# Optimization experiments

Hardware: AMD Instinct MI355X
Metric: run time of the kernel (lower is better)

The kernel has to match this reference:

```python
import jax, jax.numpy as jnp
import numpy as np

N = 32768          # flattened tokens
D = 256            # latent_dim
K = 8192           # codebook_size
COMMIT_W = 0.25    # commitment_weight


def setup_inputs() -> dict:
    key = jax.random.key(0)
    k1, k2, k3 = jax.random.split(key, 3)
    x = jax.random.normal(k1, (N, D), dtype=jnp.float32)
    # nn.init.uniform_(embedding.weight, -1/K, 1/K)
    embedding = jax.random.uniform(k2, (K, D), dtype=jnp.float32,
                                   minval=-1.0 / K, maxval=1.0 / K)
    # out_proj: Linear(D, D, bias=False); torch default kaiming-uniform ~ U(-1/sqrt(D), 1/sqrt(D))
    lim = 1.0 / np.sqrt(D)
    w_out = jax.random.uniform(k3, (D, D), dtype=jnp.float32, minval=-lim, maxval=lim)
    return {"x": x, "embedding": embedding, "w_out": w_out}


def reference(x, embedding, w_out):
    sg = jax.lax.stop_gradient
    # codebook = out_proj(embedding.weight)  -> [K, D]
    codebook = embedding @ w_out.T
    # torch.cdist(x, codebook, p=2) is only consumed by argmin, so squared
    # Euclidean distances give the identical ids without the sqrt.
    x2 = jnp.sum(x * x, axis=1, keepdims=True)          # [N, 1]
    c2 = jnp.sum(codebook * codebook, axis=1)           # [K]
    dists = x2 - 2.0 * (x @ codebook.T) + c2            # [N, K]
    ids = jnp.argmin(dists, axis=1)                     # [N]
    q = codebook[ids]                                   # [N, D] gather
    # straight-through estimator
    quantized = x + sg(q - x)
    loss = jnp.mean((x - sg(quantized)) ** 2) \
         + COMMIT_W * jnp.mean((quantized - sg(x)) ** 2)
    return quantized, ids, loss
```

## Files before the change

kernel.cpp:

```cpp
#include <hip/hip_runtime.h>
#include <hip/hip_bf16.h>

#define N_TOK 32768
#define DIM   256
#define KCB   8192
#define CAP   64
#define MARGIN 1.75e-4f

typedef __attribute__((ext_vector_type(8))) short short8v;
typedef __attribute__((ext_vector_type(4))) float f32x4;

__device__ __forceinline__ unsigned int mono_f32(float f) {
    unsigned int u = __float_as_uint(f);
    return (u >> 31) ? ~u : (u | 0x80000000u);
}
__device__ __forceinline__ float invmono_f32(unsigned int m) {
    unsigned int u = (m & 0x80000000u) ? (m & 0x7FFFFFFFu) : ~m;
    return __uint_as_float(u);
}
__device__ __forceinline__ unsigned long long shfl_xor_u64(unsigned long long v, int m) {
    unsigned int lo = (unsigned int)v, hi = (unsigned int)(v >> 32);
    lo = __shfl_xor(lo, m, 64);
    hi = __shfl_xor(hi, m, 64);
    return ((unsigned long long)hi << 32) | lo;
}
__device__ __forceinline__ void gl_lds16(const void* g, void* l) {
    __builtin_amdgcn_global_load_lds(
        (const __attribute__((address_space(1))) unsigned int*)g,
        (__attribute__((address_space(3))) unsigned int*)l, 16, 0, 0);
}
__device__ __forceinline__ unsigned int rne16(float f) {
    unsigned int b = __float_as_uint(f);
    return (b + 0x7FFFu + ((b >> 16) & 1u)) >> 16;
}

__global__ __launch_bounds__(256) void transpose_w(const float* __restrict__ w,
                                                   float* __restrict__ wT) {
    __shared__ float tile[32][33];
    int bx = blockIdx.x & 7, by = blockIdx.x >> 3;
    int x0 = bx * 32, y0 = by * 32;
    int tx = threadIdx.x & 31, ty = threadIdx.x >> 5;
    #pragma unroll
    for (int i = 0; i < 32; i += 8)
        tile[ty + i][tx] = w[(y0 + ty + i) * DIM + x0 + tx];
    __syncthreads();
    #pragma unroll
    for (int i = 0; i < 32; i += 8)
        wT[(x0 + ty + i) * DIM + y0 + tx] = tile[tx][ty + i];
}

#define KPB 8
__global__ __launch_bounds__(256) void build_codebook(const float* __restrict__ emb,
                                                      const float* __restrict__ wT,
                                                      float* __restrict__ cb) {
    __shared__ float e[KPB][DIM];
    const int k0 = blockIdx.x * KPB;
    const int t = threadIdx.x;
    for (int i = t; i < KPB * DIM / 4; i += 256)
        ((float4*)&e[0][0])[i] = ((const float4*)(emb + (size_t)k0 * DIM))[i];
    __syncthreads();
    const int d = t;
    float acc[KPB];
    #pragma unroll
    for (int kk = 0; kk < KPB; ++kk) acc[kk] = 0.f;
    for (int j = 0; j < DIM; ++j) {
        float w = wT[j * DIM + d];
        #pragma unroll
        for (int kk = 0; kk < KPB; ++kk)
            acc[kk] = fmaf(e[kk][j], w, acc[kk]);
    }
    #pragma unroll
    for (int kk = 0; kk < KPB; ++kk)
        cb[(size_t)(k0 + kk) * DIM + d] = acc[kk];
}

__global__ __launch_bounds__(256) void sumsq_np_bf(const float* __restrict__ a,
                                                   float* __restrict__ out,
                                                   uint4* __restrict__ bfout) {
    #pragma clang fp contract(off)
    int idx = blockIdx.x * 256 + threadIdx.x;
    int r = idx >> 1, h = idx & 1;
    const float* b = a + (size_t)r * DIM + h * 128;
    uint4* dst = bfout ? bfout + ((size_t)r * 32 + h * 16) : (uint4*)0;
    float r0 = 0.f, r1 = 0.f, r2 = 0.f, r3 = 0.f,
          r4 = 0.f, r5 = 0.f, r6 = 0.f, r7 = 0.f;
    #pragma unroll
    for (int i = 0; i < 128; i += 8) {
        float4 p = *(const float4*)(b + i);
        float4 q = *(const float4*)(b + i + 4);
        if (bfout) {
            uint4 u;
            u.x = rne16(p.x) | (rne16(p.y) << 16);
            u.y = rne16(p.z) | (rne16(p.w) << 16);
            u.z = rne16(q.x) | (rne16(q.y) << 16);
            u.w = rne16(q.z) | (rne16(q.w) << 16);
            dst[i >> 3] = u;
        }
        r0 = r0 + p.x * p.x; r1 = r1 + p.y * p.y;
        r2 = r2 + p.z * p.z; r3 = r3 + p.w * p.w;
        r4 = r4 + q.x * q.x; r5 = r5 + q.y * q.y;
        r6 = r6 + q.z * q.z; r7 = r7 + q.w * q.w;
    }
    float half = ((r0 + r1) + (r2 + r3)) + ((r4 + r5) + (r6 + r7));
    float other = __shfl_xor(half, 1, 64);
    if (h == 0) out[r] = half + other;
}

__global__ __launch_bounds__(512, 2) void score_collect(
    const unsigned short* __restrict__ xbf,
    const unsigned short* __restrict__ cbbf,
    unsigned int* __restrict__ gmax,
    unsigned int* __restrict__ ccnt,
    unsigned short* __restrict__ cand)
{
    __shared__ unsigned char lds[131072];
    __shared__ float auxm[2][256];
    const int t = threadIdx.x;
    const int l = t & 63, w = t >> 6;
    const int g = l >> 4, c = l & 15;
    const int wr = w >> 1, wc = w & 1;
    const int row0 = blockIdx.x * 256;
    const int col0 = blockIdx.y * 256;

    f32x4 acc[4][8];
    #pragma unroll
    for (int m = 0; m < 4; ++m)
        #pragma unroll
        for (int n = 0; n < 8; ++n) acc[m][n] = (f32x4){0.f, 0.f, 0.f, 0.f};

    const char* xg = (const char*)xbf  + (size_t)row0 * 512;
    const char* cg = (const char*)cbbf + (size_t)col0 * 512;

#define STAGE(buf, ks)                                                         \
    do {                                                                       \
        const int kb_ = (ks) * 128;                                            \
        unsigned char* la_ = lds + (buf) * 65536;                              \
        _Pragma("unroll")                                                      \
        for (int r_ = 0; r_ < 4; ++r_) {            \
            int i_ = r_ * 512 + t;                                             \
            int row_ = i_ >> 3, pc_ = i_ & 7;                                  \
            gl_lds16(xg + (size_t)row_ * 512 + kb_ + ((pc_ ^ (row_ & 7)) * 16),\
                     la_ + i_ * 16);                                           \
        }                                                                      \
        _Pragma("unroll")                                                      \
        for (int r_ = 0; r_ < 4; ++r_) {            \
            int i_ = r_ * 512 + t;                                             \
            int row_ = i_ >> 3, pc_ = i_ & 7;                                  \
            gl_lds16(cg + (size_t)row_ * 512 + kb_ + ((pc_ ^ (row_ & 7)) * 16),\
                     la_ + 32768 + i_ * 16);                                   \
        }                                                                      \
    } while (0)

    STAGE(0, 0);
    asm volatile("s_waitcnt vmcnt(0)" ::: "memory");
    __syncthreads();

    int cur = 0;
    #pragma unroll
    for (int ks = 0; ks < 4; ++ks) {
        if (ks < 3) STAGE(cur ^ 1, ks + 1);
        const unsigned char* la = lds + cur * 65536;
        const unsigned char* lb = la + 32768;
        #pragma unroll
        for (int kk = 0; kk < 2; ++kk) {
            const int sw = ((kk * 4 + g) ^ (c & 7)) * 16;
            short8v af[4], bv[8];
            #pragma unroll
            for (int m = 0; m < 4; ++m)
                af[m] = *(const short8v*)(la + (64 * wr + 16 * m + c) * 128 + sw);
            #pragma unroll
            for (int n = 0; n < 8; ++n)
                bv[n] = *(const short8v*)(lb + (128 * wc + 16 * n + c) * 128 + sw);
            #pragma unroll
            for (int m = 0; m < 4; ++m)
                #pragma unroll
                for (int n = 0; n < 8; ++n)
                    acc[m][n] = __builtin_amdgcn_mfma_f32_16x16x32_bf16(
                        af[m], bv[n], acc[m][n], 0, 0, 0);
        }
        asm volatile("s_waitcnt vmcnt(0)" ::: "memory");
        __syncthreads();
        cur ^= 1;
    }
#undef STAGE

    #pragma unroll
    for (int m = 0; m < 4; ++m)
        #pragma unroll
        for (int j = 0; j < 4; ++j) {
            float v = acc[m][0][j];
            #pragma unroll
            for (int n = 1; n < 8; ++n) v = fmaxf(v, acc[m][n][j]);
            #pragma unroll
            for (int msk = 1; msk < 16; msk <<= 1)
                v = fmaxf(v, __shfl_xor(v, msk, 64));
            if (c == 0) auxm[wc][64 * wr + 16 * m + 4 * g + j] = v;
        }
    __syncthreads();

    if (wc == 0 && c == 0) {
        float vm[16];
        unsigned int ou[16];
        #pragma unroll
        for (int i = 0; i < 16; ++i) {
            int row = 64 * wr + 16 * (i >> 2) + 4 * g + (i & 3);
            vm[i] = fmaxf(auxm[0][row], auxm[1][row]);
        }
        #pragma unroll
        for (int i = 0; i < 16; ++i) {
            int row = 64 * wr + 16 * (i >> 2) + 4 * g + (i & 3);
            ou[i] = atomicMax(&gmax[row0 + row], mono_f32(vm[i]));
        }
        #pragma unroll
        for (int i = 0; i < 16; ++i) {
            int row = 64 * wr + 16 * (i >> 2) + 4 * g + (i & 3);
            auxm[0][row] = fmaxf(vm[i], invmono_f32(ou[i]));
        }
    }
    __syncthreads();

    #pragma unroll
    for (int m = 0; m < 4; ++m)
        #pragma unroll
        for (int j = 0; j < 4; ++j) {
            int lrow = 64 * wr + 16 * m + 4 * g + j;
            float thr = auxm[0][lrow] - MARGIN;
            #pragma unroll
            for (int n = 0; n < 8; ++n) {
                float s = acc[m][n][j];
                if (s >= thr) {
                    int row = row0 + lrow;
                    unsigned int idx = atomicAdd(&ccnt[row], 1u);
                    if (idx < CAP)
                        cand[((size_t)row << 6) + idx] =
                            (unsigned short)(col0 + 128 * wc + 16 * n + c);
                }
            }
        }
}

__device__ __forceinline__ unsigned long long np_dist_pack(
    const float4* __restrict__ xr4, const float* __restrict__ cb,
    int k, float X2, const float* __restrict__ c2)
{
    #pragma clang fp contract(off)
    const float4* cr4 = (const float4*)(cb + (size_t)k * DIM);
    float a = 0.f;
    #pragma unroll 8
    for (int t4 = 0; t4 < DIM / 4; ++t4) {
        float4 xv = xr4[t4];
        float4 cv = cr4[t4];
        a = fmaf(xv.x, cv.x, a);
        a = fmaf(xv.y, cv.y, a);
        a = fmaf(xv.z, cv.z, a);
        a = fmaf(xv.w, cv.w, a);
    }
    float u  = X2 - 2.0f * a;
    float dd = u + c2[k];
    return ((unsigned long long)mono_f32(dd) << 32) | (unsigned int)k;
}

__global__ __launch_bounds__(256) void exact_select(
    const float* __restrict__ x, const float* __restrict__ cb,
    const float* __restrict__ x2, const float* __restrict__ c2,
    const unsigned int* __restrict__ ccnt, const unsigned short* __restrict__ cand,
    unsigned long long* __restrict__ best)
{
    const int l = threadIdx.x & 63;
    const int row = (blockIdx.x * 256 + threadIdx.x) >> 6;
    const unsigned int cnt = ccnt[row];
    const float4* xr4 = (const float4*)(x + (size_t)row * DIM);
    const float X2 = x2[row];
    unsigned long long bp = ~0ull;

    if (cnt <= CAP) {
        if (l < (int)cnt) {
            int k = (int)cand[((size_t)row << 6) + l];
            bp = np_dist_pack(xr4, cb, k, X2, c2);
        }
    } else {
        for (int k = l; k < KCB; k += 64) {
            unsigned long long pk = np_dist_pack(xr4, cb, k, X2, c2);
            if (pk < bp) bp = pk;
        }
    }
    #pragma unroll
    for (int m = 1; m < 64; m <<= 1) {
        unsigned long long v = shfl_xor_u64(bp, m);
        if (v < bp) bp = v;
    }
    if (l == 0) best[row] = bp;
}

__global__ __launch_bounds__(256, 4) void score_argmin(const float* __restrict__ x,
                                                       const float* __restrict__ cb,
                                                       const float* __restrict__ c2,
                                                       const float* __restrict__ x2,
                                                       unsigned long long* __restrict__ best) {
    #pragma clang fp contract(off)
    __shared__ float As[16][128];
    __shared__ float Bs[16][128];
    const int row0 = blockIdx.x * 128;
    const int col0 = blockIdx.y * 128;
    const int t = threadIdx.x;
    const int tn = t & 15, tm = t >> 4;
    const int lrow = t >> 1, lseg = (t & 1) * 4;
    float acc[8][8];
    #pragma unroll
    for (int i = 0; i < 8; ++i)
        #pragma unroll
        for (int j = 0; j < 8; ++j) acc[i][j] = 0.f;
    const float* xp = x  + (size_t)(row0 + lrow) * DIM + lseg;
    const float* cp = cb + (size_t)(col0 + lrow) * DIM + lseg;
    for (int k0 = 0; k0 < DIM; k0 += 16) {
        float4 a0 = *(const float4*)(xp + k0);
        float4 a1 = *(const float4*)(xp + k0 + 8);
        float4 b0 = *(const float4*)(cp + k0);
        float4 b1 = *(const float4*)(cp + k0 + 8);
        __syncthreads();
        As[lseg + 0][lrow] = a0.x; As[lseg + 1][lrow] = a0.y;
        As[lseg + 2][lrow] = a0.z; As[lseg + 3][lrow] = a0.w;
        As[8 + lseg + 0][lrow] = a1.x; As[8 + lseg + 1][lrow] = a1.y;
        As[8 + lseg + 2][lrow] = a1.z; As[8 + lseg + 3][lrow] = a1.w;
        Bs[lseg + 0][lrow] = b0.x; Bs[lseg + 1][lrow] = b0.y;
        Bs[lseg + 2][lrow] = b0.z; Bs[lseg + 3][lrow] = b0.w;
        Bs[8 + lseg + 0][lrow] = b1.x; Bs[8 + lseg + 1][lrow] = b1.y;
        Bs[8 + lseg + 2][lrow] = b1.z; Bs[8 + lseg + 3][lrow] = b1.w;
        __syncthreads();
        #pragma unroll
        for (int kk = 0; kk < 16; ++kk) {
            float a[8], b[8];
            *(float4*)(a)     = *(const float4*)&As[kk][tm * 4];
            *(float4*)(a + 4) = *(const float4*)&As[kk][64 + tm * 4];
            *(float4*)(b)     = *(const float4*)&Bs[kk][tn * 4];
            *(float4*)(b + 4) = *(const float4*)&Bs[kk][64 + tn * 4];
            #pragma unroll
            for (int i = 0; i < 8; ++i)
                #pragma unroll
                for (int j = 0; j < 8; ++j)
                    acc[i][j] = fmaf(a[i], b[j], acc[i][j]);
        }
    }
    float c2v[8], x2v[8];
    #pragma unroll
    for (int j = 0; j < 4; ++j) {
        c2v[j]     = c2[col0 + tn * 4 + j];
        c2v[4 + j] = c2[col0 + 64 + tn * 4 + j];
    }
    #pragma unroll
    for (int i = 0; i < 4; ++i) {
        x2v[i]     = x2[row0 + tm * 4 + i];
        x2v[4 + i] = x2[row0 + 64 + tm * 4 + i];
    }
    #pragma unroll
    for (int i = 0; i < 8; ++i) {
        unsigned long long bp = ~0ull;
        #pragma unroll
        for (int j = 0; j < 8; ++j) {
            float tt = 2.0f * acc[i][j];
            float u  = x2v[i] - tt;
            float dd = u + c2v[j];
            int id = col0 + ((j < 4) ? (tn * 4 + j) : (64 + tn * 4 + (j - 4)));
            unsigned long long pk = ((unsigned long long)mono_f32(dd) << 32) | (unsigned int)id;
            if (pk < bp) bp = pk;
        }
        #pragma unroll
        for (int m = 1; m < 16; m <<= 1) {
            unsigned long long v = shfl_xor_u64(bp, m);
            if (v < bp) bp = v;
        }
        if (tn == 0) {
            int gr = row0 + ((i < 4) ? (tm * 4 + i) : (64 + tm * 4 + (i - 4)));
            atomicMin(&best[gr], bp);
        }
    }
}

__global__ __launch_bounds__(256) void finalize(const float* __restrict__ x,
                                                const float* __restrict__ cb,
                                                const unsigned long long* __restrict__ best,
                                                float* __restrict__ out,
                                                float* __restrict__ partial) {
    const int r = blockIdx.x;
    const int d = threadIdx.x;
    const int id = (int)(best[r] & 0xFFFFFFFFu);
    const float q  = cb[(size_t)id * DIM + d];
    const float xv = x[(size_t)r * DIM + d];
    out[(size_t)r * DIM + d] = q;
    float df = xv - q;
    float v = df * df;
    #pragma unroll
    for (int o = 32; o > 0; o >>= 1) v += __shfl_down(v, o, 64);
    __shared__ float w4[4];
    if ((d & 63) == 0) w4[d >> 6] = v;
    __syncthreads();
    if (d == 0) {
        partial[r] = w4[0] + w4[1] + w4[2] + w4[3];
        out[(size_t)N_TOK * DIM + r] = (float)id;
    }
}

__global__ __launch_bounds__(256) void reduce_loss(const float* __restrict__ partial,
                                                   float* __restrict__ out) {
    float s = 0.f;
    for (int i = threadIdx.x; i < N_TOK / 4; i += 256) {
        float4 v = ((const float4*)partial)[i];
        s += (v.x + v.y) + (v.z + v.w);
    }
    #pragma unroll
    for (int o = 32; o > 0; o >>= 1) s += __shfl_down(s, o, 64);
    __shared__ float w4[4];
    if ((threadIdx.x & 63) == 0) w4[threadIdx.x >> 6] = s;
    __syncthreads();
    if (threadIdx.x == 0)
        out[(size_t)N_TOK * DIM + N_TOK] =
            (w4[0] + w4[1] + w4[2] + w4[3]) * (1.25f / ((float)N_TOK * (float)DIM));
}

extern "C" void kernel_launch(void* const* d_in, const int* in_sizes, int n_in,
                              void* d_out, int out_size, void* d_ws, size_t ws_size,
                              hipStream_t stream) {
    const float* x     = (const float*)d_in[0];
    const float* emb   = (const float*)d_in[1];
    const float* w_out = (const float*)d_in[2];
    float* out = (float*)d_out;

    char* ws = (char*)d_ws;
    unsigned long long* best = (unsigned long long*)ws;
    float* x2 = (float*)(ws + 262400);
    float* wT = (float*)(ws + 393472);
    float* cb = (float*)(ws + 655616);
    float* c2 = (float*)(ws + 9044224);
    unsigned int*   gmax = (unsigned int*)(ws + 9076992);
    unsigned int*   ccnt = (unsigned int*)(ws + 9208064);
    unsigned short* cand = (unsigned short*)(ws + 9339136);
    unsigned short* xbf  = (unsigned short*)(ws + 13533440);
    unsigned short* cbbf = (unsigned short*)(ws + 30310656);
    float* partial = wT;
    const size_t NEED = 34504960;
    const bool useMfma = (ws_size >= NEED);

    transpose_w   <<<64,  256, 0, stream>>>(w_out, wT);
    build_codebook<<<KCB / KPB, 256, 0, stream>>>(emb, wT, cb);
    sumsq_np_bf   <<<N_TOK * 2 / 256, 256, 0, stream>>>(x, x2,
                      useMfma ? (uint4*)xbf : (uint4*)0);
    sumsq_np_bf   <<<KCB * 2 / 256, 256, 0, stream>>>(cb, c2,
                      useMfma ? (uint4*)cbbf : (uint4*)0);

    if (useMfma) {
        hipMemsetAsync(gmax, 0, 262144, stream);
        score_collect <<<dim3(N_TOK / 256, KCB / 256), 512, 0, stream>>>(
            xbf, cbbf, gmax, ccnt, cand);
        exact_select  <<<N_TOK / 4, 256, 0, stream>>>(x, cb, x2, c2, ccnt, cand, best);
    } else {
        hipMemsetAsync(best, 0xFF, 262144, stream);
        score_argmin  <<<dim3(N_TOK / 128, KCB / 128), 256, 0, stream>>>(x, cb, c2, x2, best);
    }

    finalize      <<<N_TOK, 256, 0, stream>>>(x, cb, best, out, partial);
    reduce_loss   <<<1, 256, 0, stream>>>(partial, out);
}
```

Measured before the change: 525.1 us.

## Switch GEMM K-loop to 4-stage LDS ring with partial vmcnt waits

```diff
diff --git a/kernel.cpp b/kernel.cpp
--- a/kernel.cpp
+++ b/kernel.cpp
@@ -131,56 +131,60 @@
     const char* xg = (const char*)xbf  + (size_t)row0 * 512;
     const char* cg = (const char*)cbbf + (size_t)col0 * 512;
 
-#define STAGE(buf, ks)                                                         \
+#define STAGE(b_, s_)                                                          \
     do {                                                                       \
-        const int kb_ = (ks) * 128;                                            \
-        unsigned char* la_ = lds + (buf) * 65536;                              \
+        const int kb_ = (s_) * 64;                                             \
+        unsigned char* la_ = lds + (b_) * 32768;                               \
         _Pragma("unroll")                                                      \
-        for (int r_ = 0; r_ < 4; ++r_) {            \
+        for (int r_ = 0; r_ < 2; ++r_) {           \
             int i_ = r_ * 512 + t;                                             \
-            int row_ = i_ >> 3, pc_ = i_ & 7;                                  \
-            gl_lds16(xg + (size_t)row_ * 512 + kb_ + ((pc_ ^ (row_ & 7)) * 16),\
+            int row_ = i_ >> 2, pc_ = i_ & 3;                                  \
+            int sz_ = (row_ ^ (row_ >> 2)) & 3;                                \
+            gl_lds16(xg + (size_t)row_ * 512 + kb_ + ((pc_ ^ sz_) * 16),       \
                      la_ + i_ * 16);                                           \
         }                                                                      \
         _Pragma("unroll")                                                      \
-        for (int r_ = 0; r_ < 4; ++r_) {            \
+        for (int r_ = 0; r_ < 2; ++r_) {           \
             int i_ = r_ * 512 + t;                                             \
-            int row_ = i_ >> 3, pc_ = i_ & 7;                                  \
-            gl_lds16(cg + (size_t)row_ * 512 + kb_ + ((pc_ ^ (row_ & 7)) * 16),\
-                     la_ + 32768 + i_ * 16);                                   \
+            int row_ = i_ >> 2, pc_ = i_ & 3;                                  \
+            int sz_ = (row_ ^ (row_ >> 2)) & 3;                                \
+            gl_lds16(cg + (size_t)row_ * 512 + kb_ + ((pc_ ^ sz_) * 16),       \
+                     la_ + 16384 + i_ * 16);                                   \
         }                                                                      \
     } while (0)
 
-    STAGE(0, 0);
-    asm volatile("s_waitcnt vmcnt(0)" ::: "memory");
-    __syncthreads();
-
-    int cur = 0;
-    #pragma unroll
-    for (int ks = 0; ks < 4; ++ks) {
-        if (ks < 3) STAGE(cur ^ 1, ks + 1);
-        const unsigned char* la = lds + cur * 65536;
-        const unsigned char* lb = la + 32768;
-        #pragma unroll
-        for (int kk = 0; kk < 2; ++kk) {
-            const int sw = ((kk * 4 + g) ^ (c & 7)) * 16;
-            short8v af[4], bv[8];
-            #pragma unroll
-            for (int m = 0; m < 4; ++m)
-                af[m] = *(const short8v*)(la + (64 * wr + 16 * m + c) * 128 + sw);
+    const int swq = (g ^ (c & 3) ^ ((c >> 2) & 3)) * 16;
+
+    STAGE(0, 0); STAGE(1, 1); STAGE(2, 2);
+    asm volatile("s_waitcnt vmcnt(8)" ::: "memory");
+    __builtin_amdgcn_s_barrier();
+    asm volatile("" ::: "memory");
+
+    #pragma unroll
+    for (int s = 0; s < 8; ++s) {
+        if (s < 5) STAGE((s + 3) & 3, s + 3);
+        const unsigned char* la = lds + (s & 3) * 32768;
+        const unsigned char* lb = la + 16384;
+        short8v af[4], bv[8];
+        #pragma unroll
+        for (int m = 0; m < 4; ++m)
+            af[m] = *(const short8v*)(la + (64 * wr + 16 * m + c) * 64 + swq);
+        #pragma unroll
+        for (int n = 0; n < 8; ++n)
+            bv[n] = *(const short8v*)(lb + (128 * wc + 16 * n + c) * 64 + swq);
+        #pragma unroll
+        for (int m = 0; m < 4; ++m)
             #pragma unroll
             for (int n = 0; n < 8; ++n)
-                bv[n] = *(const short8v*)(lb + (128 * wc + 16 * n + c) * 128 + sw);
-            #pragma unroll
-            for (int m = 0; m < 4; ++m)
-                #pragma unroll
-                for (int n = 0; n < 8; ++n)
-                    acc[m][n] = __builtin_amdgcn_mfma_f32_16x16x32_bf16(
-                        af[m], bv[n], acc[m][n], 0, 0, 0);
-        }
-        asm volatile("s_waitcnt vmcnt(0)" ::: "memory");
-        __syncthreads();
-        cur ^= 1;
+                acc[m][n] = __builtin_amdgcn_mfma_f32_16x16x32_bf16(
+                    af[m], bv[n], acc[m][n], 0, 0, 0);
+        if (s < 7) {
+            if (s <= 4)      asm volatile("s_waitcnt vmcnt(8)" ::: "memory");
+            else if (s == 5) asm volatile("s_waitcnt vmcnt(4)" ::: "memory");
+            else             asm volatile("s_waitcnt vmcnt(0)" ::: "memory");
+            __builtin_amdgcn_s_barrier();
+            asm volatile("" ::: "memory");
+        }
     }
 #undef STAGE
 
```

Measured after the change: 536.0 us. +2.1%, slower.
